# Kernel tuning notes

Measured on AMD Instinct MI355X. Metric: run time of the kernel, lower is better.

Reference implementation:

```python
import jax, jax.numpy as jnp
import numpy as np

N_NODES = 30000
N_EDGES = 480000
EMB_DIM = 512
NUM_REL = 4
VOCAB = 64


def setup_inputs() -> dict:
    key = jax.random.key(0)
    ks = jax.random.split(key, 14)

    def nrm(k, shape):
        return jax.random.normal(k, shape, dtype=jnp.float32) * 0.05

    return {
        "x_idx": jax.random.randint(ks[0], (N_NODES, 1), 0, VOCAB),
        "edge_index": jax.random.randint(ks[1], (2, N_EDGES), 0, N_NODES),
        "edge_type": jax.random.randint(ks[2], (N_EDGES,), 0, NUM_REL),
        "emb": nrm(ks[3], (VOCAB, EMB_DIM)),
        "W1": nrm(ks[4], (NUM_REL, EMB_DIM, EMB_DIM)),
        "root1": nrm(ks[5], (EMB_DIM, EMB_DIM)),
        "b1": jnp.zeros((EMB_DIM,), jnp.float32),
        "W2": nrm(ks[6], (NUM_REL, EMB_DIM, EMB_DIM)),
        "root2": nrm(ks[7], (EMB_DIM, EMB_DIM)),
        "b2": jnp.zeros((EMB_DIM,), jnp.float32),
        "W3": nrm(ks[8], (NUM_REL, EMB_DIM, EMB_DIM)),
        "root3": nrm(ks[9], (EMB_DIM, EMB_DIM)),
        "b3": jnp.zeros((EMB_DIM,), jnp.float32),
    }


def rgcn_conv(x, src, dst, etype, W, Wroot, b):
    # PyG RGCNConv semantics: per-relation MEAN aggregation of neighbor
    # features, transformed by relation weight, plus root transform + bias.
    # Aggregate-then-transform is mathematically identical to per-edge
    # transform (mean is linear) but needs only R dense GEMMs.
    R = W.shape[0]
    Nn, Dd = x.shape
    seg = etype * Nn + dst  # combined (relation, dst) segment id
    msg_sum = jax.ops.segment_sum(x[src], seg, num_segments=R * Nn)
    msg_sum = msg_sum.reshape(R, Nn, Dd)  # [R, N, D]
    cnt = jax.ops.segment_sum(jnp.ones((src.shape[0],), x.dtype), seg,
                              num_segments=R * Nn).reshape(R, Nn, 1)
    mean = msg_sum / jnp.maximum(cnt, 1.0)  # zero rows stay zero
    out = jnp.einsum('rnd,rde->ne', mean, W)  # relation-specific transform
    return out + x @ Wroot + b


def reference(x_idx, edge_index, edge_type, emb,
              W1, root1, b1, W2, root2, b2, W3, root3, b3):
    src, dst = edge_index[0], edge_index[1]
    x = emb[x_idx[:, 0]]  # [N, D] embedding lookup (squeeze(-1))
    x = jax.nn.relu(rgcn_conv(x, src, dst, edge_type, W1, root1, b1)) + x
    x = jax.nn.relu(rgcn_conv(x, src, dst, edge_type, W2, root2, b2)) + x
    x = jax.nn.relu(rgcn_conv(x, src, dst, edge_type, W3, root3, b3)) + x
    return x
```

## Files before the change

kernel.cpp:

```cpp
#include <hip/hip_runtime.h>
#include <hip/hip_bf16.h>

#define N_NODES 30000
#define N_EDGES 480000
#define DIM 512
#define NREL 4
#define NSEG (NREL * N_NODES)
#define KTOT ((NREL + 1) * DIM)
#define NT (KTOT / 64)
#define NBM ((N_NODES + 255) / 256)
#define NWG_GEMM (NBM * 2)

typedef __attribute__((ext_vector_type(8))) short short8;
typedef __attribute__((ext_vector_type(4))) float f32x4;

__device__ __forceinline__ float bf2f(unsigned int hi) {
    union { unsigned int u; float f; } v; v.u = hi << 16; return v.f;
}
__device__ __forceinline__ unsigned short f2bf(float f) {
    union { float f; unsigned int u; } v; v.f = f;
    unsigned int u = v.u;
    unsigned int r = (u + 0x7fffu + ((u >> 16) & 1u)) >> 16;
    return (unsigned short)r;
}

__global__ void k_wcat(const float* __restrict__ W, const float* __restrict__ root,
                       unsigned short* __restrict__ wt) {
    int i = blockIdx.x * 256 + threadIdx.x;
    if (i >= DIM * KTOT) return;
    int k = i % KTOT, e = i / KTOT;
    float v;
    if (k < DIM) {
        v = root[k * DIM + e];
    } else {
        int kk = k - DIM;
        int r = kk >> 9; kk &= 511;
        v = W[(size_t)r * DIM * DIM + (size_t)kk * DIM + e];
    }
    wt[(size_t)e * KTOT + k] = f2bf(v);
}

__global__ void k_embed(const int* __restrict__ xidx, const float* __restrict__ emb,
                        unsigned short* __restrict__ xb) {
    int n = blockIdx.x;
    int l = threadIdx.x;
    int id = xidx[n];
    const float4* er = (const float4*)(emb + (size_t)id * DIM + l * 8);
    float4 a = er[0], b = er[1];
    ushort4 pa, pb;
    pa.x = f2bf(a.x); pa.y = f2bf(a.y); pa.z = f2bf(a.z); pa.w = f2bf(a.w);
    pb.x = f2bf(b.x); pb.y = f2bf(b.y); pb.z = f2bf(b.z); pb.w = f2bf(b.w);
    ushort4* xbo = (ushort4*)(xb + (size_t)n * DIM + l * 8);
    xbo[0] = pa; xbo[1] = pb;
}

__global__ void k_hist(const int* __restrict__ etype, const int* __restrict__ dst,
                       int* __restrict__ hist) {
    int e = blockIdx.x * 256 + threadIdx.x;
    if (e < N_EDGES) atomicAdd(&hist[etype[e] * N_NODES + dst[e]], 1);
}

__global__ void k_scan1(const int* __restrict__ hist, int* __restrict__ offsets,
                        int* __restrict__ bsums) {
    __shared__ int sdata[256];
    int t = threadIdx.x, b = blockIdx.x;
    int base = b * 2048 + t * 8;
    int v[8]; int s = 0;
    #pragma unroll
    for (int i = 0; i < 8; i++) {
        int idx = base + i;
        v[i] = (idx < NSEG) ? hist[idx] : 0;
        s += v[i];
    }
    sdata[t] = s; __syncthreads();
    for (int off = 1; off < 256; off <<= 1) {
        int x = (t >= off) ? sdata[t - off] : 0;
        __syncthreads();
        sdata[t] += x;
        __syncthreads();
    }
    int run = (t == 0) ? 0 : sdata[t - 1];
    #pragma unroll
    for (int i = 0; i < 8; i++) {
        run += v[i];
        int idx = base + i;
        if (idx < NSEG) offsets[idx + 1] = run;
    }
    if (t == 255) bsums[b] = sdata[255];
}

__global__ void k_scan2(int* __restrict__ bsums, int nb) {
    if (threadIdx.x == 0 && blockIdx.x == 0) {
        int run = 0;
        for (int i = 0; i < nb; i++) { int v = bsums[i]; bsums[i] = run; run += v; }
    }
}

__global__ void k_scan3(const int* __restrict__ bsums, int* __restrict__ offsets) {
    int t = threadIdx.x, b = blockIdx.x;
    int base = b * 2048 + t * 8;
    int add = bsums[b];
    #pragma unroll
    for (int i = 0; i < 8; i++) {
        int idx = base + i;
        if (idx < NSEG) offsets[idx + 1] += add;
    }
    if (b == 0 && t == 0) offsets[0] = 0;
}

__global__ void k_scatter(const int* __restrict__ etype, const int* __restrict__ src,
                          const int* __restrict__ dst, const int* __restrict__ offsets,
                          int* __restrict__ cursor, int* __restrict__ ssrc) {
    int e = blockIdx.x * 256 + threadIdx.x;
    if (e < N_EDGES) {
        int seg = etype[e] * N_NODES + dst[e];
        int p = atomicAdd(&cursor[seg], 1);
        ssrc[offsets[seg] + p] = src[e];
    }
}

__global__ __launch_bounds__(256) void k_agg(const unsigned short* __restrict__ xb,
                                             const int* __restrict__ ssrc,
                                             const int* __restrict__ offsets,
                                             unsigned short* __restrict__ meanb) {
    int wid = threadIdx.x >> 6, lane = threadIdx.x & 63;
    int seg = blockIdx.x * 4 + wid;
    int st = offsets[seg], en = offsets[seg + 1];
    float acc[8] = {0, 0, 0, 0, 0, 0, 0, 0};
    int i = st;
    for (; i + 1 < en; i += 2) {
        int s0 = ssrc[i], s1 = ssrc[i + 1];
        uint4 v0 = *(const uint4*)(xb + (size_t)s0 * DIM + lane * 8);
        uint4 v1 = *(const uint4*)(xb + (size_t)s1 * DIM + lane * 8);
        acc[0] += bf2f(v0.x & 0xffffu) + bf2f(v1.x & 0xffffu);
        acc[1] += bf2f(v0.x >> 16)     + bf2f(v1.x >> 16);
        acc[2] += bf2f(v0.y & 0xffffu) + bf2f(v1.y & 0xffffu);
        acc[3] += bf2f(v0.y >> 16)     + bf2f(v1.y >> 16);
        acc[4] += bf2f(v0.z & 0xffffu) + bf2f(v1.z & 0xffffu);
        acc[5] += bf2f(v0.z >> 16)     + bf2f(v1.z >> 16);
        acc[6] += bf2f(v0.w & 0xffffu) + bf2f(v1.w & 0xffffu);
        acc[7] += bf2f(v0.w >> 16)     + bf2f(v1.w >> 16);
    }
    if (i < en) {
        int s = ssrc[i];
        uint4 v = *(const uint4*)(xb + (size_t)s * DIM + lane * 8);
        acc[0] += bf2f(v.x & 0xffffu); acc[1] += bf2f(v.x >> 16);
        acc[2] += bf2f(v.y & 0xffffu); acc[3] += bf2f(v.y >> 16);
        acc[4] += bf2f(v.z & 0xffffu); acc[5] += bf2f(v.z >> 16);
        acc[6] += bf2f(v.w & 0xffffu); acc[7] += bf2f(v.w >> 16);
    }
    float inv = (en > st) ? 1.0f / (float)(en - st) : 0.0f;
    uint4 o;
    o.x = (unsigned int)f2bf(acc[0] * inv) | ((unsigned int)f2bf(acc[1] * inv) << 16);
    o.y = (unsigned int)f2bf(acc[2] * inv) | ((unsigned int)f2bf(acc[3] * inv) << 16);
    o.z = (unsigned int)f2bf(acc[4] * inv) | ((unsigned int)f2bf(acc[5] * inv) << 16);
    o.w = (unsigned int)f2bf(acc[6] * inv) | ((unsigned int)f2bf(acc[7] * inv) << 16);
    *(uint4*)(meanb + (size_t)seg * DIM + lane * 8) = o;
}


#define GLD16(g, l)                                                                     \
    __builtin_amdgcn_global_load_lds((const __attribute__((address_space(1))) void*)(g), \
                                     (__attribute__((address_space(3))) void*)(l), 16, 0, 0)

#define STAGE_A(tile, ksh, bufo) do {                                                   \
    int _pt = (tile) >> 3;                                                              \
    const unsigned short* _ab = (_pt == 0) ? xb : meanb + (size_t)(_pt - 1) * N_NODES * DIM; \
    int _kc = (((tile) & 7) << 6) + ((ksh) << 5) + gcol;         \
    int _g0 = m0 + srow; if (_g0 >= N_NODES) _g0 = 0;                                   \
    int _g1 = m0 + srow + 128; if (_g1 >= N_NODES) _g1 = 0;                             \
    GLD16(_ab + (size_t)_g0 * DIM + _kc, S + (bufo) + ((ksh) * 8192) + (wid << 9));     \
    GLD16(_ab + (size_t)_g1 * DIM + _kc, S + (bufo) + ((ksh) * 8192) + 4096 + (wid << 9)); \
} while (0)

#define STAGE_B(tile, ksh, bufo) do {                                                   \
    int _kc = ((tile) << 6) + ((ksh) << 5) + gcol;                  \
    const unsigned short* _w0 = wt + (size_t)(n0 + srow) * KTOT + _kc;                  \
    GLD16(_w0, S + (bufo) + 16384 + ((ksh) * 8192) + (wid << 9));                       \
    GLD16(_w0 + (size_t)128 * KTOT, S + (bufo) + 16384 + ((ksh) * 8192) + 4096 + (wid << 9)); \
} while (0)

#define READ_A8(ks, bufo) do {                                                          \
    const unsigned short* _ap = S + (bufo) + (ks) * 8192 + arowF + cofs;                \
    a[0] = *(const short8*)(_ap);                                                       \
    a[1] = *(const short8*)(_ap + 512);                                                 \
    a[2] = *(const short8*)(_ap + 1024);                                                \
    a[3] = *(const short8*)(_ap + 1536);                                                \
    a[4] = *(const short8*)(_ap + 2048);                                                \
    a[5] = *(const short8*)(_ap + 2560);                                                \
    a[6] = *(const short8*)(_ap + 3072);                                                \
    a[7] = *(const short8*)(_ap + 3584);                                                \
} while (0)

#define READ_B(ks, bufo) do {                                                           \
    const unsigned short* _bp = S + (bufo) + 16384 + (ks) * 8192 + brow0 + cofs;        \
    b[0] = *(const short8*)(_bp);                                                       \
    b[1] = *(const short8*)(_bp + 512);                                                 \
    b[2] = *(const short8*)(_bp + 1024);                                                \
    b[3] = *(const short8*)(_bp + 1536);                                                \
} while (0)

#define MFMA32() do {                                                                   \
    _Pragma("unroll") for (int _m = 0; _m < 8; ++_m)                                    \
    _Pragma("unroll") for (int _n = 0; _n < 4; ++_n)                                    \
        acc[_m][_n] =                                                                   \
            __builtin_amdgcn_mfma_f32_16x16x32_bf16(a[_m], b[_n], acc[_m][_n], 0, 0, 0); \
} while (0)

#define PH_TOP()  __builtin_amdgcn_s_barrier();                                         \
                  asm volatile("s_waitcnt lgkmcnt(0)" ::: "memory");                    \
                  __builtin_amdgcn_sched_barrier(0);                                    \
                  __builtin_amdgcn_s_setprio(1)
#define PH_BOT()  __builtin_amdgcn_s_setprio(0); __builtin_amdgcn_sched_barrier(0);     \
                  __builtin_amdgcn_s_barrier()
#define VMC4()    asm volatile("s_waitcnt vmcnt(4)" ::: "memory")
#define VMC0()    asm volatile("s_waitcnt vmcnt(0)" ::: "memory")
#define BUF1 32768

__global__ __launch_bounds__(512, 2) void k_gemm(const unsigned short* __restrict__ xb,
                                                 const unsigned short* __restrict__ meanb,
                                                 const unsigned short* __restrict__ wt,
                                                 const float* __restrict__ bias,
                                                 float* __restrict__ outf,
                                                 unsigned short* __restrict__ xbn,
                                                 int wf32, int wbf16) {
    extern __shared__ unsigned short S[];
    int tid = threadIdx.x;
    int lane = tid & 63, wid = tid >> 6;

    int orig = blockIdx.x;
    int xcd = orig & 7, tix = orig >> 3;
    const int q = NWG_GEMM >> 3, r = NWG_GEMM & 7;
    int wgid = (xcd < r ? xcd * (q + 1) : r * (q + 1) + (xcd - r) * q) + tix;
    int bn = wgid & 1, bm = wgid >> 1;
    int m0 = bm * 256, n0 = bn * 256;
    int wm = wid >> 2, wn = wid & 3;

    int r15 = lane & 15, c4 = lane >> 4;
    int f = (r15 + (r15 >> 2)) & 3;
    int cofs = ((c4 ^ f) << 3);
    int arowF = (wm * 128 + r15) * 32;
    int brow0 = (wn * 64 + r15) * 32;

    int srow = tid >> 2;
    int f_t = (srow + (srow >> 2)) & 3;
    int gcol = (((tid & 3) ^ f_t) << 3);

    short8 a[8], b[4];
    f32x4 acc[8][4] = {};

    STAGE_A(0, 0, 0);    STAGE_B(0, 0, 0);
    STAGE_A(0, 1, 0);    STAGE_B(0, 1, 0);
    STAGE_A(1, 0, BUF1); STAGE_B(1, 0, BUF1);
    VMC4();
    __builtin_amdgcn_s_barrier();

    for (int it = 0; it < NT / 2; ++it) {
        int t1 = 2 * it + 1, t2 = 2 * it + 2, t3 = 2 * it + 3;
        READ_A8(0, 0); READ_B(0, 0);
        STAGE_A(t1, 1, BUF1); STAGE_B(t1, 1, BUF1);
        PH_TOP(); MFMA32(); PH_BOT();
        READ_A8(1, 0); READ_B(1, 0);
        if (t2 < NT) { STAGE_A(t2, 0, 0); STAGE_B(t2, 0, 0); VMC4(); } else { VMC0(); }
        PH_TOP(); MFMA32(); PH_BOT();
        READ_A8(0, BUF1); READ_B(0, BUF1);
        if (t2 < NT) { STAGE_A(t2, 1, 0); STAGE_B(t2, 1, 0); }
        PH_TOP(); MFMA32(); PH_BOT();
        READ_A8(1, BUF1); READ_B(1, BUF1);
        if (t3 < NT) { STAGE_A(t3, 0, BUF1); STAGE_B(t3, 0, BUF1); VMC4(); } else { VMC0(); }
        PH_TOP(); MFMA32(); PH_BOT();
    }
    VMC0();

    #pragma unroll
    for (int mm = 0; mm < 8; ++mm) {
        int rowoff = ((mm >> 2) << 6) + ((mm & 3) << 4);
        #pragma unroll
        for (int j = 0; j < 4; ++j) {
            int row = m0 + wm * 128 + rowoff + c4 * 4 + j;
            if (row >= N_NODES) continue;
            #pragma unroll
            for (int n = 0; n < 4; ++n) {
                int col = n0 + wn * 64 + n * 16 + r15;
                float v = acc[mm][n][j] + bias[col];
                v = fmaxf(v, 0.0f) + bf2f(xb[(size_t)row * DIM + col]);
                if (wf32)  outf[(size_t)row * DIM + col] = v;
                if (wbf16) xbn[(size_t)row * DIM + col] = f2bf(v);
            }
        }
    }
}

extern "C" void kernel_launch(void* const* d_in, const int* in_sizes, int n_in,
                              void* d_out, int out_size, void* d_ws, size_t ws_size,
                              hipStream_t stream) {
    const int* xidx   = (const int*)d_in[0];
    const int* eidx   = (const int*)d_in[1];
    const int* etype  = (const int*)d_in[2];
    const float* emb  = (const float*)d_in[3];
    const float* Wl[3]    = {(const float*)d_in[4], (const float*)d_in[7], (const float*)d_in[10]};
    const float* rootl[3] = {(const float*)d_in[5], (const float*)d_in[8], (const float*)d_in[11]};
    const float* bl[3]    = {(const float*)d_in[6], (const float*)d_in[9], (const float*)d_in[12]};
    const int* esrc = eidx;
    const int* edst = eidx + N_EDGES;

    char* ws = (char*)d_ws;
    size_t off = 0;
    auto take = [&](size_t bytes) { char* p = ws + off; off = (off + bytes + 255) & ~(size_t)255; return p; };
    unsigned short* xb0  = (unsigned short*)take((size_t)N_NODES * DIM * 2);
    unsigned short* xb1  = (unsigned short*)take((size_t)N_NODES * DIM * 2);
    unsigned short* meanb= (unsigned short*)take((size_t)NREL * N_NODES * DIM * 2);
    unsigned short* wcat = (unsigned short*)take((size_t)3 * DIM * KTOT * 2);
    int* hist    = (int*)take((size_t)NSEG * 4);
    int* offsets = (int*)take((size_t)(NSEG + 1) * 4);
    int* cursor  = (int*)take((size_t)NSEG * 4);
    int* bsums   = (int*)take(64 * 4);
    int* ssrc    = (int*)take((size_t)N_EDGES * 4);

    hipMemsetAsync(hist, 0, (size_t)NSEG * 4, stream);
    hipMemsetAsync(cursor, 0, (size_t)NSEG * 4, stream);
    for (int l = 0; l < 3; l++) {
        k_wcat<<<(DIM * KTOT + 255) / 256, 256, 0, stream>>>(Wl[l], rootl[l],
                                                             wcat + (size_t)l * DIM * KTOT);
    }
    k_embed<<<N_NODES, 64, 0, stream>>>(xidx, emb, xb0);
    k_hist<<<(N_EDGES + 255) / 256, 256, 0, stream>>>(etype, edst, hist);
    k_scan1<<<(NSEG + 2047) / 2048, 256, 0, stream>>>(hist, offsets, bsums);
    k_scan2<<<1, 64, 0, stream>>>(bsums, (NSEG + 2047) / 2048);
    k_scan3<<<(NSEG + 2047) / 2048, 256, 0, stream>>>(bsums, offsets);
    k_scatter<<<(N_EDGES + 255) / 256, 256, 0, stream>>>(etype, esrc, edst, offsets, cursor, ssrc);

    unsigned short* xb_cur = xb0;
    unsigned short* xb_nxt = xb1;
    for (int l = 0; l < 3; l++) {
        k_agg<<<N_NODES, 256, 0, stream>>>(xb_cur, ssrc, offsets, meanb);
        int last = (l == 2);
        k_gemm<<<NWG_GEMM, 512, 131072, stream>>>(xb_cur, meanb, wcat + (size_t)l * DIM * KTOT,
                                                  bl[l], (float*)d_out, xb_nxt,
                                                  last ? 1 : 0, last ? 0 : 1);
        unsigned short* t = xb_cur; xb_cur = xb_nxt; xb_nxt = t;
    }
}
```

Baseline: 659.1 us.

## Split GEMM inner loop into half-tile phases with LDS register double-buffering

Restructures the GEMM main loop so each k-substep is split into two half-M MFMA phases (16 MFMAs each). The LDS reads for the next phase go into alternate register sets (a0/a1, rb0/rb1) and are issued before the barrier. The explicit lgkmcnt(0) wait is removed from the phase top, and global staging of A and B is interleaved across the finer phases with adjusted vmcnt waits. The goal is to overlap LDS reads and global loads with MFMA work. The cost is twice as many barriers, and the memory-ordering assumptions around the removed LDS wait are riskier.

```diff
diff --git a/kernel.cpp b/kernel.cpp
--- a/kernel.cpp
+++ b/kernel.cpp
@@ -180,39 +180,34 @@
     GLD16(_w0 + (size_t)128 * KTOT, S + (bufo) + 16384 + ((ksh) * 8192) + 4096 + (wid << 9)); \
 } while (0)
 
-#define READ_A8(ks, bufo) do {                                                          \
-    const unsigned short* _ap = S + (bufo) + (ks) * 8192 + arowF + cofs;                \
-    a[0] = *(const short8*)(_ap);                                                       \
-    a[1] = *(const short8*)(_ap + 512);                                                 \
-    a[2] = *(const short8*)(_ap + 1024);                                                \
-    a[3] = *(const short8*)(_ap + 1536);                                                \
-    a[4] = *(const short8*)(_ap + 2048);                                                \
-    a[5] = *(const short8*)(_ap + 2560);                                                \
-    a[6] = *(const short8*)(_ap + 3072);                                                \
-    a[7] = *(const short8*)(_ap + 3584);                                                \
-} while (0)
-
-#define READ_B(ks, bufo) do {                                                           \
+#define RD_A(dst, ks, mq, bufo) do {                                                    \
+    const unsigned short* _ap = S + (bufo) + (ks) * 8192 + arowF + (mq) * 2048 + cofs;  \
+    dst[0] = *(const short8*)(_ap);                                                     \
+    dst[1] = *(const short8*)(_ap + 512);                                               \
+    dst[2] = *(const short8*)(_ap + 1024);                                              \
+    dst[3] = *(const short8*)(_ap + 1536);                                              \
+} while (0)
+
+#define RD_B(dst, ks, bufo) do {                                                        \
     const unsigned short* _bp = S + (bufo) + 16384 + (ks) * 8192 + brow0 + cofs;        \
-    b[0] = *(const short8*)(_bp);                                                       \
-    b[1] = *(const short8*)(_bp + 512);                                                 \
-    b[2] = *(const short8*)(_bp + 1024);                                                \
-    b[3] = *(const short8*)(_bp + 1536);                                                \
-} while (0)
-
-#define MFMA32() do {                                                                   \
-    _Pragma("unroll") for (int _m = 0; _m < 8; ++_m)                                    \
+    dst[0] = *(const short8*)(_bp);                                                     \
+    dst[1] = *(const short8*)(_bp + 512);                                               \
+    dst[2] = *(const short8*)(_bp + 1024);                                              \
+    dst[3] = *(const short8*)(_bp + 1536);                                              \
+} while (0)
+
+#define MFMAH(av, bv, h) do {                                                           \
+    _Pragma("unroll") for (int _m = 0; _m < 4; ++_m)                                    \
     _Pragma("unroll") for (int _n = 0; _n < 4; ++_n)                                    \
-        acc[_m][_n] =                                                                   \
-            __builtin_amdgcn_mfma_f32_16x16x32_bf16(a[_m], b[_n], acc[_m][_n], 0, 0, 0); \
-} while (0)
-
-#define PH_TOP()  __builtin_amdgcn_s_barrier();                                         \
-                  asm volatile("s_waitcnt lgkmcnt(0)" ::: "memory");                    \
-                  __builtin_amdgcn_sched_barrier(0);                                    \
+        acc[(h) * 4 + _m][_n] =                                                         \
+            __builtin_amdgcn_mfma_f32_16x16x32_bf16(av[_m], bv[_n], acc[(h) * 4 + _m][_n], 0, 0, 0); \
+} while (0)
+
+#define PH_TOP()  __builtin_amdgcn_s_barrier(); __builtin_amdgcn_sched_barrier(0);      \
                   __builtin_amdgcn_s_setprio(1)
 #define PH_BOT()  __builtin_amdgcn_s_setprio(0); __builtin_amdgcn_sched_barrier(0);     \
                   __builtin_amdgcn_s_barrier()
+#define VMC6()    asm volatile("s_waitcnt vmcnt(6)" ::: "memory")
 #define VMC4()    asm volatile("s_waitcnt vmcnt(4)" ::: "memory")
 #define VMC0()    asm volatile("s_waitcnt vmcnt(0)" ::: "memory")
 #define BUF1 32768
@@ -246,29 +241,42 @@
     int f_t = (srow + (srow >> 2)) & 3;
     int gcol = (((tid & 3) ^ f_t) << 3);
 
-    short8 a[8], b[4];
+    short8 a0[4], a1[4], rb0[4], rb1[4];
     f32x4 acc[8][4] = {};
 
-    STAGE_A(0, 0, 0);    STAGE_B(0, 0, 0);
-    STAGE_A(0, 1, 0);    STAGE_B(0, 1, 0);
-    STAGE_A(1, 0, BUF1); STAGE_B(1, 0, BUF1);
-    VMC4();
+    STAGE_B(0, 0, 0); STAGE_A(0, 0, 0); STAGE_B(0, 1, 0); STAGE_A(0, 1, 0);
+    STAGE_B(1, 0, BUF1); STAGE_A(1, 0, BUF1); STAGE_B(1, 1, BUF1);
+    VMC6();
     __builtin_amdgcn_s_barrier();
+    __builtin_amdgcn_sched_barrier(0);
+    RD_A(a0, 0, 0, 0); RD_B(rb0, 0, 0);
 
     for (int it = 0; it < NT / 2; ++it) {
         int t1 = 2 * it + 1, t2 = 2 * it + 2, t3 = 2 * it + 3;
-        READ_A8(0, 0); READ_B(0, 0);
-        STAGE_A(t1, 1, BUF1); STAGE_B(t1, 1, BUF1);
-        PH_TOP(); MFMA32(); PH_BOT();
-        READ_A8(1, 0); READ_B(1, 0);
-        if (t2 < NT) { STAGE_A(t2, 0, 0); STAGE_B(t2, 0, 0); VMC4(); } else { VMC0(); }
-        PH_TOP(); MFMA32(); PH_BOT();
-        READ_A8(0, BUF1); READ_B(0, BUF1);
-        if (t2 < NT) { STAGE_A(t2, 1, 0); STAGE_B(t2, 1, 0); }
-        PH_TOP(); MFMA32(); PH_BOT();
-        READ_A8(1, BUF1); READ_B(1, BUF1);
-        if (t3 < NT) { STAGE_A(t3, 0, BUF1); STAGE_B(t3, 0, BUF1); VMC4(); } else { VMC0(); }
-        PH_TOP(); MFMA32(); PH_BOT();
+        RD_A(a1, 0, 1, 0);
+        STAGE_A(t1, 1, BUF1);
+        PH_TOP(); MFMAH(a0, rb0, 0); PH_BOT();
+        RD_A(a0, 1, 0, 0); RD_B(rb1, 1, 0);
+        if (t2 < NT) STAGE_B(t2, 0, 0);
+        PH_TOP(); MFMAH(a1, rb0, 1); PH_BOT();
+        RD_A(a1, 1, 1, 0);
+        if (t2 < NT) { STAGE_A(t2, 0, 0); VMC4(); } else { VMC0(); }
+        PH_TOP(); MFMAH(a0, rb1, 0); PH_BOT();
+        RD_A(a0, 0, 0, BUF1); RD_B(rb0, 0, BUF1);
+        if (t2 < NT) STAGE_B(t2, 1, 0);
+        PH_TOP(); MFMAH(a1, rb1, 1); PH_BOT();
+        RD_A(a1, 0, 1, BUF1);
+        if (t2 < NT) STAGE_A(t2, 1, 0);
+        PH_TOP(); MFMAH(a0, rb0, 0); PH_BOT();
+        RD_A(a0, 1, 0, BUF1); RD_B(rb1, 1, BUF1);
+        if (t3 < NT) STAGE_B(t3, 0, BUF1);
+        PH_TOP(); MFMAH(a1, rb0, 1); PH_BOT();
+        RD_A(a1, 1, 1, BUF1);
+        if (t3 < NT) { STAGE_A(t3, 0, BUF1); VMC4(); } else { VMC0(); }
+        PH_TOP(); MFMAH(a0, rb1, 0); PH_BOT();
+        if (t2 < NT) { RD_A(a0, 0, 0, 0); RD_B(rb0, 0, 0); }
+        if (t3 < NT) STAGE_B(t3, 1, BUF1);
+        PH_TOP(); MFMAH(a1, rb1, 1); PH_BOT();
     }
     VMC0();
 
```

New measurement: 754.4 us. +14.5%, slower.

## Retile GEMM to 128x128 with 256-thread workgroups and restructured LDS pipeline

Applied to the files above, without the earlier changes.

The fused relation/root GEMM moves from 256x256 tiles on 512-thread workgroups to 128x128 tiles on 256-thread workgroups. This raises the workgroup count from roughly one per CU to several, so all CUs get work and the tail is smaller. The LDS staging is reworked to a smaller double buffer with per-half-tile prefetch, and the trailing barrier in each phase is dropped. The cost is less operand reuse per tile and a tighter synchronisation pattern. The embedding kernel now packs four nodes per block, and the two workspace memsets are merged into one by making the buffers adjacent.

```diff
diff --git a/kernel.cpp b/kernel.cpp
--- a/kernel.cpp
+++ b/kernel.cpp
@@ -8,8 +8,8 @@
 #define NSEG (NREL * N_NODES)
 #define KTOT ((NREL + 1) * DIM)
 #define NT (KTOT / 64)
-#define NBM ((N_NODES + 255) / 256)
-#define NWG_GEMM (NBM * 2)
+#define NBM ((N_NODES + 127) / 128)
+#define NWG_GEMM (NBM * 4)
 
 typedef __attribute__((ext_vector_type(8))) short short8;
 typedef __attribute__((ext_vector_type(4))) float f32x4;
@@ -42,8 +42,9 @@
 
 __global__ void k_embed(const int* __restrict__ xidx, const float* __restrict__ emb,
                         unsigned short* __restrict__ xb) {
-    int n = blockIdx.x;
-    int l = threadIdx.x;
+    int n = blockIdx.x * 4 + (threadIdx.x >> 6);
+    int l = threadIdx.x & 63;
+    if (n >= N_NODES) return;
     int id = xidx[n];
     const float4* er = (const float4*)(emb + (size_t)id * DIM + l * 8);
     float4 a = er[0], b = er[1];
@@ -168,40 +169,36 @@
     const unsigned short* _ab = (_pt == 0) ? xb : meanb + (size_t)(_pt - 1) * N_NODES * DIM; \
     int _kc = (((tile) & 7) << 6) + ((ksh) << 5) + gcol;         \
     int _g0 = m0 + srow; if (_g0 >= N_NODES) _g0 = 0;                                   \
-    int _g1 = m0 + srow + 128; if (_g1 >= N_NODES) _g1 = 0;                             \
-    GLD16(_ab + (size_t)_g0 * DIM + _kc, S + (bufo) + ((ksh) * 8192) + (wid << 9));     \
-    GLD16(_ab + (size_t)_g1 * DIM + _kc, S + (bufo) + ((ksh) * 8192) + 4096 + (wid << 9)); \
+    int _g1 = m0 + srow + 64; if (_g1 >= N_NODES) _g1 = 0;                              \
+    GLD16(_ab + (size_t)_g0 * DIM + _kc, S + (bufo) + ((ksh) << 12) + (wid << 9));      \
+    GLD16(_ab + (size_t)_g1 * DIM + _kc, S + (bufo) + ((ksh) << 12) + 2048 + (wid << 9)); \
 } while (0)
 
 #define STAGE_B(tile, ksh, bufo) do {                                                   \
     int _kc = ((tile) << 6) + ((ksh) << 5) + gcol;                  \
     const unsigned short* _w0 = wt + (size_t)(n0 + srow) * KTOT + _kc;                  \
-    GLD16(_w0, S + (bufo) + 16384 + ((ksh) * 8192) + (wid << 9));                       \
-    GLD16(_w0 + (size_t)128 * KTOT, S + (bufo) + 16384 + ((ksh) * 8192) + 4096 + (wid << 9)); \
-} while (0)
-
-#define READ_A8(ks, bufo) do {                                                          \
-    const unsigned short* _ap = S + (bufo) + (ks) * 8192 + arowF + cofs;                \
+    GLD16(_w0, S + (bufo) + 8192 + ((ksh) << 12) + (wid << 9));                         \
+    GLD16(_w0 + (size_t)64 * KTOT, S + (bufo) + 8192 + ((ksh) << 12) + 2048 + (wid << 9)); \
+} while (0)
+
+#define READ_A(ks, bufo) do {                                                           \
+    const unsigned short* _ap = S + (bufo) + ((ks) << 12) + arowF + cofs;               \
     a[0] = *(const short8*)(_ap);                                                       \
     a[1] = *(const short8*)(_ap + 512);                                                 \
     a[2] = *(const short8*)(_ap + 1024);                                                \
     a[3] = *(const short8*)(_ap + 1536);                                                \
-    a[4] = *(const short8*)(_ap + 2048);                                                \
-    a[5] = *(const short8*)(_ap + 2560);                                                \
-    a[6] = *(const short8*)(_ap + 3072);                                                \
-    a[7] = *(const short8*)(_ap + 3584);                                                \
 } while (0)
 
 #define READ_B(ks, bufo) do {                                                           \
-    const unsigned short* _bp = S + (bufo) + 16384 + (ks) * 8192 + brow0 + cofs;        \
+    const unsigned short* _bp = S + (bufo) + 8192 + ((ks) << 12) + brow0 + cofs;        \
     b[0] = *(const short8*)(_bp);                                                       \
     b[1] = *(const short8*)(_bp + 512);                                                 \
     b[2] = *(const short8*)(_bp + 1024);                                                \
     b[3] = *(const short8*)(_bp + 1536);                                                \
 } while (0)
 
-#define MFMA32() do {                                                                   \
-    _Pragma("unroll") for (int _m = 0; _m < 8; ++_m)                                    \
+#define MFMA16() do {                                                                   \
+    _Pragma("unroll") for (int _m = 0; _m < 4; ++_m)                                    \
     _Pragma("unroll") for (int _n = 0; _n < 4; ++_n)                                    \
         acc[_m][_n] =                                                                   \
             __builtin_amdgcn_mfma_f32_16x16x32_bf16(a[_m], b[_n], acc[_m][_n], 0, 0, 0); \
@@ -211,13 +208,12 @@
                   asm volatile("s_waitcnt lgkmcnt(0)" ::: "memory");                    \
                   __builtin_amdgcn_sched_barrier(0);                                    \
                   __builtin_amdgcn_s_setprio(1)
-#define PH_BOT()  __builtin_amdgcn_s_setprio(0); __builtin_amdgcn_sched_barrier(0);     \
-                  __builtin_amdgcn_s_barrier()
+#define PH_BOT()  __builtin_amdgcn_s_setprio(0); __builtin_amdgcn_sched_barrier(0)
 #define VMC4()    asm volatile("s_waitcnt vmcnt(4)" ::: "memory")
 #define VMC0()    asm volatile("s_waitcnt vmcnt(0)" ::: "memory")
-#define BUF1 32768
-
-__global__ __launch_bounds__(512, 2) void k_gemm(const unsigned short* __restrict__ xb,
+#define BUF1 16384
+
+__global__ __launch_bounds__(256, 2) void k_gemm(const unsigned short* __restrict__ xb,
                                                  const unsigned short* __restrict__ meanb,
                                                  const unsigned short* __restrict__ wt,
                                                  const float* __restrict__ bias,
@@ -232,57 +228,56 @@
     int xcd = orig & 7, tix = orig >> 3;
     const int q = NWG_GEMM >> 3, r = NWG_GEMM & 7;
     int wgid = (xcd < r ? xcd * (q + 1) : r * (q + 1) + (xcd - r) * q) + tix;
-    int bn = wgid & 1, bm = wgid >> 1;
-    int m0 = bm * 256, n0 = bn * 256;
-    int wm = wid >> 2, wn = wid & 3;
+    int bn = wgid & 3, bm = wgid >> 2;
+    int m0 = bm * 128, n0 = bn * 128;
+    int wm = wid >> 1, wn = wid & 1;
 
     int r15 = lane & 15, c4 = lane >> 4;
     int f = (r15 + (r15 >> 2)) & 3;
     int cofs = ((c4 ^ f) << 3);
-    int arowF = (wm * 128 + r15) * 32;
+    int arowF = (wm * 64 + r15) * 32;
     int brow0 = (wn * 64 + r15) * 32;
 
-    int srow = tid >> 2;
+    int srow = (wid << 4) + (lane >> 2);
     int f_t = (srow + (srow >> 2)) & 3;
-    int gcol = (((tid & 3) ^ f_t) << 3);
-
-    short8 a[8], b[4];
-    f32x4 acc[8][4] = {};
-
-    STAGE_A(0, 0, 0);    STAGE_B(0, 0, 0);
-    STAGE_A(0, 1, 0);    STAGE_B(0, 1, 0);
-    STAGE_A(1, 0, BUF1); STAGE_B(1, 0, BUF1);
-    VMC4();
+    int gcol = (((lane & 3) ^ f_t) << 3);
+
+    short8 a[4], b[4];
+    f32x4 acc[4][4] = {};
+
+    STAGE_A(0, 0, 0); STAGE_B(0, 0, 0); STAGE_A(0, 1, 0); STAGE_B(0, 1, 0);
+    VMC0();
     __builtin_amdgcn_s_barrier();
 
     for (int it = 0; it < NT / 2; ++it) {
-        int t1 = 2 * it + 1, t2 = 2 * it + 2, t3 = 2 * it + 3;
-        READ_A8(0, 0); READ_B(0, 0);
+        int t1 = 2 * it + 1, t2 = 2 * it + 2;
+        READ_A(0, 0); READ_B(0, 0);
+        STAGE_A(t1, 0, BUF1); STAGE_B(t1, 0, BUF1);
+        VMC4();
+        PH_TOP(); MFMA16(); PH_BOT();
+        READ_A(1, 0); READ_B(1, 0);
         STAGE_A(t1, 1, BUF1); STAGE_B(t1, 1, BUF1);
-        PH_TOP(); MFMA32(); PH_BOT();
-        READ_A8(1, 0); READ_B(1, 0);
+        VMC4();
+        PH_TOP(); MFMA16(); PH_BOT();
+        READ_A(0, BUF1); READ_B(0, BUF1);
         if (t2 < NT) { STAGE_A(t2, 0, 0); STAGE_B(t2, 0, 0); VMC4(); } else { VMC0(); }
-        PH_TOP(); MFMA32(); PH_BOT();
-        READ_A8(0, BUF1); READ_B(0, BUF1);
-        if (t2 < NT) { STAGE_A(t2, 1, 0); STAGE_B(t2, 1, 0); }
-        PH_TOP(); MFMA32(); PH_BOT();
-        READ_A8(1, BUF1); READ_B(1, BUF1);
-        if (t3 < NT) { STAGE_A(t3, 0, BUF1); STAGE_B(t3, 0, BUF1); VMC4(); } else { VMC0(); }
-        PH_TOP(); MFMA32(); PH_BOT();
+        PH_TOP(); MFMA16(); PH_BOT();
+        READ_A(1, BUF1); READ_B(1, BUF1);
+        if (t2 < NT) { STAGE_A(t2, 1, 0); STAGE_B(t2, 1, 0); VMC4(); } else { VMC0(); }
+        PH_TOP(); MFMA16(); PH_BOT();
     }
     VMC0();
 
     #pragma unroll
-    for (int mm = 0; mm < 8; ++mm) {
-        int rowoff = ((mm >> 2) << 6) + ((mm & 3) << 4);
+    for (int m = 0; m < 4; ++m) {
         #pragma unroll
         for (int j = 0; j < 4; ++j) {
-            int row = m0 + wm * 128 + rowoff + c4 * 4 + j;
+            int row = m0 + wm * 64 + m * 16 + c4 * 4 + j;
             if (row >= N_NODES) continue;
             #pragma unroll
             for (int n = 0; n < 4; ++n) {
                 int col = n0 + wn * 64 + n * 16 + r15;
-                float v = acc[mm][n][j] + bias[col];
+                float v = acc[m][n][j] + bias[col];
                 v = fmaxf(v, 0.0f) + bf2f(xb[(size_t)row * DIM + col]);
                 if (wf32)  outf[(size_t)row * DIM + col] = v;
                 if (wbf16) xbn[(size_t)row * DIM + col] = f2bf(v);
@@ -312,18 +307,17 @@
     unsigned short* meanb= (unsigned short*)take((size_t)NREL * N_NODES * DIM * 2);
     unsigned short* wcat = (unsigned short*)take((size_t)3 * DIM * KTOT * 2);
     int* hist    = (int*)take((size_t)NSEG * 4);
+    int* cursor  = (int*)take((size_t)NSEG * 4);
     int* offsets = (int*)take((size_t)(NSEG + 1) * 4);
-    int* cursor  = (int*)take((size_t)NSEG * 4);
     int* bsums   = (int*)take(64 * 4);
     int* ssrc    = (int*)take((size_t)N_EDGES * 4);
 
-    hipMemsetAsync(hist, 0, (size_t)NSEG * 4, stream);
-    hipMemsetAsync(cursor, 0, (size_t)NSEG * 4, stream);
+    hipMemsetAsync(hist, 0, (size_t)2 * NSEG * 4, stream);
     for (int l = 0; l < 3; l++) {
         k_wcat<<<(DIM * KTOT + 255) / 256, 256, 0, stream>>>(Wl[l], rootl[l],
                                                              wcat + (size_t)l * DIM * KTOT);
     }
-    k_embed<<<N_NODES, 64, 0, stream>>>(xidx, emb, xb0);
+    k_embed<<<(N_NODES + 3) / 4, 256, 0, stream>>>(xidx, emb, xb0);
     k_hist<<<(N_EDGES + 255) / 256, 256, 0, stream>>>(etype, edst, hist);
     k_scan1<<<(NSEG + 2047) / 2048, 256, 0, stream>>>(hist, offsets, bsums);
     k_scan2<<<1, 64, 0, stream>>>(bsums, (NSEG + 2047) / 2048);
@@ -335,9 +329,9 @@
     for (int l = 0; l < 3; l++) {
         k_agg<<<N_NODES, 256, 0, stream>>>(xb_cur, ssrc, offsets, meanb);
         int last = (l == 2);
-        k_gemm<<<NWG_GEMM, 512, 131072, stream>>>(xb_cur, meanb, wcat + (size_t)l * DIM * KTOT,
-                                                  bl[l], (float*)d_out, xb_nxt,
-                                                  last ? 1 : 0, last ? 0 : 1);
+        k_gemm<<<NWG_GEMM, 256, 65536, stream>>>(xb_cur, meanb, wcat + (size_t)l * DIM * KTOT,
+                                                 bl[l], (float*)d_out, xb_nxt,
+                                                 last ? 1 : 0, last ? 0 : 1);
         unsigned short* t = xb_cur; xb_cur = xb_nxt; xb_nxt = t;
     }
 }
```

Result: slower. 685.1 us (+3.9%).
